# Performance work log

Measured on AMD Instinct MI355X. Metric: run time of the kernel, lower is better.

The kernel has to match this reference:

```python
import jax, jax.numpy as jnp
import numpy as np
import itertools

N_SUBSETS = 4
TAU = 0.1


def setup_inputs() -> dict:
    key = jax.random.key(0)
    k1, k2, k3 = jax.random.split(key, 3)
    # scale projections so exp(sim/tau) stays numerically sane (module assumes small/normalized projections)
    projections = jax.random.normal(k1, (8192, 128), dtype=jnp.float32) * 0.05
    xrecon = jax.random.normal(k2, (8192, 784), dtype=jnp.float32)
    recon_label = jax.random.normal(k3, (8192, 784), dtype=jnp.float32)
    return {"projections": projections, "xrecon": xrecon, "recon_label": recon_label}


def _joint_loss(projections, xrecon, recon_label):
    # reconstruction MSE
    recon_loss = jnp.mean(jnp.square(xrecon - recon_label))

    # ---- XNegloss (SimCLR-style with n_subsets positives per group) ----
    N, D = projections.shape
    sim = (projections @ projections.T) / TAU  # [N, N] dot similarity
    gid = jnp.arange(N) // N_SUBSETS
    pos_mask = gid[:, None] == gid[None, :]  # same-group entries are positives
    exp_sim = jnp.exp(sim)
    # original code drops positive entries exactly equal to 1 (positives[positives != 1])
    pos_sum = jnp.sum(jnp.where(pos_mask & (sim != 1.0), exp_sim, 0.0), axis=-1)
    neg_sum = jnp.sum(jnp.where(pos_mask, 0.0, exp_sim), axis=-1)
    closs = jnp.mean(-jnp.log(pos_sum / (pos_sum + neg_sum)))

    # ---- distance loss: MSE over all subset pairs within each group ----
    combi = np.array(list(itertools.combinations(range(N_SUBSETS), 2)))
    left, right = combi[:, 0], combi[:, 1]
    P = projections.reshape(N // N_SUBSETS, N_SUBSETS, D)
    # per-group mean over (pairs, D) then mean over groups == global mean (equal counts)
    dist_loss = jnp.mean(jnp.square(P[:, left] - P[:, right]))

    loss = recon_loss + closs + dist_loss
    return loss, closs, recon_loss, dist_loss


def reference(projections, xrecon, recon_label):
    return _joint_loss(projections, xrecon, recon_label)
```

## Files before the change

### kernel.cpp

```cpp
#include <hip/hip_runtime.h>
#include <hip/hip_bf16.h>
#include <stdint.h>

typedef __bf16 bf16x8 __attribute__((ext_vector_type(8)));
typedef float  f32x4  __attribute__((ext_vector_type(4)));

#define NROWS   8192
#define DIMK    128
#define RECON_N 6422528
#define RECON_BLOCKS 1568
#define GROUP_BLOCKS 512
#define SIM_TILES    2080
#define FUSED_BLOCKS 4160

#define WS_RS     0
#define WS_G      8192
#define WS_E      16384
#define WS_RPART  24576
#define WS_DPART  26144
#define WS_PB     26656

__device__ __forceinline__ void async16(const void* g, void* l) {
    __builtin_amdgcn_global_load_lds(
        (const __attribute__((address_space(1))) void*)g,
        (__attribute__((address_space(3))) void*)l, 16, 0, 0);
}

__device__ __forceinline__ unsigned short f2bf(float f) {
    union { __hip_bfloat16 h; unsigned short u; } v;
    v.h = __float2bfloat16(f);
    return v.u;
}

__global__ __launch_bounds__(256) void prep_kernel(const float4* __restrict__ Pf,
                                                   uint2* __restrict__ Pb,
                                                   float* __restrict__ ws) {
    int idx = blockIdx.x * 256 + threadIdx.x;
    if (blockIdx.x < 32) ws[WS_RS + idx] = 0.f;
    float4 a = Pf[idx];
    uint2 r;
    r.x = (uint32_t)f2bf(a.x) | ((uint32_t)f2bf(a.y) << 16);
    r.y = (uint32_t)f2bf(a.z) | ((uint32_t)f2bf(a.w) << 16);
    Pb[idx] = r;
}

__global__ __launch_bounds__(256, 3) void fused_kernel(
        const unsigned short* __restrict__ Pb,
        const float* __restrict__ Pf,
        const float4* __restrict__ X,
        const float4* __restrict__ Y,
        float* __restrict__ ws) {
    __shared__ unsigned short tile[128 * 128];
    __shared__ float sred[2][2][64];
    __shared__ float cred[2][128];
    const int bx = blockIdx.x;
    const int wave = threadIdx.x >> 6, lane = threadIdx.x & 63;

    int role, idx;
    if (bx < 4096) {
        int r8 = bx & 7, c8 = bx >> 3;
        if ((r8 & 1) == 0)      { role = 0; idx = c8 * 4 + (r8 >> 1); }
        else if (r8 == 7)       { role = 2; idx = c8; }
        else                    { role = 1; idx = c8 * 3 + ((r8 - 1) >> 1); }
    } else if (bx < 4128) {
        role = 0; idx = 2048 + (bx - 4096);
    } else {
        role = 1; idx = 1536 + (bx - 4128);
    }

    if (role == 0) {
        float* RS = ws + WS_RS;
        float ff = 64.5f - sqrtf(64.5f * 64.5f - 2.0f * (float)idx);
        int I = (int)ff;
        int base = I * 64 - (I * (I - 1)) / 2;
        if (idx < base) { --I; base = I * 64 - (I * (I - 1)) / 2; }
        else { int nb = (I + 1) * 64 - ((I + 1) * I) / 2;
               if (idx >= nb) { ++I; base = nb; } }
        const int J = I + (idx - base);

        const int wr = wave >> 1, wc = wave & 1;
        const int m = lane & 15, kq = lane >> 4;

        const char* gB = (const char*)(Pb + (size_t)J * 128 * DIMK);
#pragma unroll
        for (int i = 0; i < 8; ++i) {
            int chunk = i * 256 + wave * 64 + lane;
            int r = chunk >> 4, qp = chunk & 15;
            async16(gB + r * 256 + (((qp - r) & 15) << 4),
                    (char*)tile + chunk * 16);
        }

        bf16x8 Af[4][4];
        const unsigned short* gA = Pb + (size_t)(I * 128 + wr * 64) * DIMK;
#pragma unroll
        for (int i = 0; i < 4; ++i) {
            const unsigned short* rowp = gA + (size_t)(i * 16 + m) * DIMK + kq * 8;
#pragma unroll
            for (int kk = 0; kk < 4; ++kk)
                Af[i][kk] = *(const bf16x8*)(rowp + kk * 32);
        }

        float rowAcc[4][4];
        float colAcc[4];
#pragma unroll
        for (int i = 0; i < 4; ++i)
#pragma unroll
            for (int r = 0; r < 4; ++r) rowAcc[i][r] = 0.f;

        __syncthreads();

#pragma unroll
        for (int j = 0; j < 4; ++j) {
            int rl = wc * 64 + j * 16 + m;
            bf16x8 Bf[4];
#pragma unroll
            for (int kk = 0; kk < 4; ++kk)
                Bf[kk] = *(const bf16x8*)((const char*)tile + rl * 256 +
                                          (((kq + kk * 4 + rl) & 15) << 4));
            f32x4 acc[4];
#pragma unroll
            for (int i = 0; i < 4; ++i) acc[i] = (f32x4){0.f, 0.f, 0.f, 0.f};
#pragma unroll
            for (int kk = 0; kk < 4; ++kk)
#pragma unroll
                for (int i = 0; i < 4; ++i)
                    acc[i] = __builtin_amdgcn_mfma_f32_16x16x32_bf16(
                        Af[i][kk], Bf[kk], acc[i], 0, 0, 0);
            float cs = 0.f;
#pragma unroll
            for (int i = 0; i < 4; ++i)
#pragma unroll
                for (int r = 0; r < 4; ++r) {
                    float e = __builtin_amdgcn_exp2f(acc[i][r] * 14.426950408889634f);
                    rowAcc[i][r] += e;
                    cs += e;
                }
            cs += __shfl_xor(cs, 16, 64);
            cs += __shfl_xor(cs, 32, 64);
            colAcc[j] = cs;
        }

#pragma unroll
        for (int i = 0; i < 4; ++i)
#pragma unroll
            for (int r = 0; r < 4; ++r) {
                float sv = rowAcc[i][r];
                sv += __shfl_xor(sv, 1, 64);
                sv += __shfl_xor(sv, 2, 64);
                sv += __shfl_xor(sv, 4, 64);
                sv += __shfl_xor(sv, 8, 64);
                rowAcc[i][r] = sv;
            }
        if (m == 0) {
#pragma unroll
            for (int i = 0; i < 4; ++i)
#pragma unroll
                for (int r = 0; r < 4; ++r)
                    sred[wc][wr][i * 16 + kq * 4 + r] = rowAcc[i][r];
        }
        if (kq == 0) {
#pragma unroll
            for (int j = 0; j < 4; ++j)
                cred[wr][wc * 64 + j * 16 + m] = colAcc[j];
        }
        __syncthreads();
        if (wc == 0) {
            float v = sred[0][wr][lane] + sred[1][wr][lane];
            atomicAdd(&RS[I * 128 + wr * 64 + lane], v);
        } else if (I != J) {
            int col = wr * 64 + lane;
            float v = cred[0][col] + cred[1][col];
            atomicAdd(&RS[J * 128 + col], v);
        }
    } else if (role == 1) {
        __shared__ float red[4];
        int base = idx * 1024 + threadIdx.x;
        float4 a0 = X[base],       b0 = Y[base];
        float4 a1 = X[base + 256], b1 = Y[base + 256];
        float4 a2 = X[base + 512], b2 = Y[base + 512];
        float4 a3 = X[base + 768], b3 = Y[base + 768];
        float s = 0.f, d;
        d = a0.x - b0.x; s += d * d;  d = a0.y - b0.y; s += d * d;
        d = a0.z - b0.z; s += d * d;  d = a0.w - b0.w; s += d * d;
        d = a1.x - b1.x; s += d * d;  d = a1.y - b1.y; s += d * d;
        d = a1.z - b1.z; s += d * d;  d = a1.w - b1.w; s += d * d;
        d = a2.x - b2.x; s += d * d;  d = a2.y - b2.y; s += d * d;
        d = a2.z - b2.z; s += d * d;  d = a2.w - b2.w; s += d * d;
        d = a3.x - b3.x; s += d * d;  d = a3.y - b3.y; s += d * d;
        d = a3.z - b3.z; s += d * d;  d = a3.w - b3.w; s += d * d;
#pragma unroll
        for (int mm = 1; mm < 64; mm <<= 1) s += __shfl_xor(s, mm, 64);
        if (lane == 0) red[wave] = s;
        __syncthreads();
        if (threadIdx.x == 0)
            ws[WS_RPART + idx] = red[0] + red[1] + red[2] + red[3];
    } else {
        __shared__ float dred[4];
        float* G = ws + WS_G;
        float* E = ws + WS_E;
        int g = idx * 4 + wave;
        const float* base = Pf + (size_t)g * 4 * DIMK;
        float v[4][2];
#pragma unroll
        for (int r = 0; r < 4; ++r) {
            v[r][0] = base[r * DIMK + lane];
            v[r][1] = base[r * DIMK + 64 + lane];
        }
        float dmat[4][4];
#pragma unroll
        for (int r = 0; r < 4; ++r)
#pragma unroll
            for (int s2 = r; s2 < 4; ++s2) {
                float p = v[r][0] * v[s2][0] + v[r][1] * v[s2][1];
#pragma unroll
                for (int mm = 1; mm < 64; mm <<= 1) p += __shfl_xor(p, mm, 64);
                dmat[r][s2] = p; dmat[s2][r] = p;
            }
        if (lane == 0) {
            float distp = 0.f;
#pragma unroll
            for (int r = 0; r < 4; ++r)
#pragma unroll
                for (int s2 = r + 1; s2 < 4; ++s2)
                    distp += dmat[r][r] + dmat[s2][s2] - 2.f * dmat[r][s2];
            dred[wave] = distp;
#pragma unroll
            for (int r = 0; r < 4; ++r) {
                float Gs = 0.f, Es = 0.f;
#pragma unroll
                for (int s2 = 0; s2 < 4; ++s2) {
                    float sim = dmat[r][s2] * 10.0f;
                    float e = __expf(sim);
                    Gs += e;
                    if (sim == 1.0f) Es += e;
                }
                G[g * 4 + r] = Gs;
                E[g * 4 + r] = Es;
            }
        }
        __syncthreads();
        if (threadIdx.x == 0)
            ws[WS_DPART + idx] = dred[0] + dred[1] + dred[2] + dred[3];
    }
}

__global__ __launch_bounds__(1024) void finalize_kernel(const float* __restrict__ ws,
                                                        float* __restrict__ out) {
    __shared__ float redc[16], redr[16], redd[16];
    const float* RS = ws + WS_RS;
    const float* G  = ws + WS_G;
    const float* E  = ws + WS_E;

    float c = 0.f;
    for (int r = threadIdx.x; r < NROWS; r += 1024) {
        float Sv = RS[r];
        c += __logf(Sv - E[r]) - __logf(G[r] - E[r]);
    }
    float rs = 0.f;
    for (int i = threadIdx.x; i < RECON_BLOCKS; i += 1024) rs += ws[WS_RPART + i];
    float ds = 0.f;
    for (int i = threadIdx.x; i < GROUP_BLOCKS; i += 1024) ds += ws[WS_DPART + i];

#pragma unroll
    for (int mm = 1; mm < 64; mm <<= 1) {
        c  += __shfl_xor(c,  mm, 64);
        rs += __shfl_xor(rs, mm, 64);
        ds += __shfl_xor(ds, mm, 64);
    }
    int wave = threadIdx.x >> 6, lane = threadIdx.x & 63;
    if (lane == 0) { redc[wave] = c; redr[wave] = rs; redd[wave] = ds; }
    __syncthreads();
    if (threadIdx.x == 0) {
        float cs = 0.f, rss = 0.f, dss = 0.f;
#pragma unroll
        for (int i = 0; i < 16; ++i) { cs += redc[i]; rss += redr[i]; dss += redd[i]; }
        float closs = cs / (float)NROWS;
        float recon = rss / (float)RECON_N;
        float dist  = dss / (float)(2048 * 6 * DIMK);
        out[0] = recon + closs + dist;
        out[1] = closs;
        out[2] = recon;
        out[3] = dist;
    }
}

extern "C" void kernel_launch(void* const* d_in, const int* in_sizes, int n_in,
                              void* d_out, int out_size, void* d_ws, size_t ws_size,
                              hipStream_t stream) {
    const float* P  = (const float*)d_in[0];
    const float4* X = (const float4*)d_in[1];
    const float4* Y = (const float4*)d_in[2];
    float* out = (float*)d_out;
    float* w = (float*)d_ws;
    unsigned short* Pb = (unsigned short*)(w + WS_PB);

    prep_kernel<<<1024, 256, 0, stream>>>((const float4*)P, (uint2*)Pb, w);
    fused_kernel<<<FUSED_BLOCKS, 256, 0, stream>>>(Pb, P, X, Y, w);
    finalize_kernel<<<1, 1024, 0, stream>>>(w, out);
}
```

Before: 129.0 us.

## Make fused kernel persistent, interleave recon loads with sim tiles, prefetch next B tile

Replaces the role-partitioned grid of 4160 blocks with a persistent grid of 1024 blocks. Each block loops over similarity tiles, streaming the reconstruction MSE loads in between MFMA steps and staging the next tile's B operand into LDS while the current tile is reduced. The group/distance work moves to the tail of blocks 512 and up. The aim is to hide the memory-bound MSE stream under the compute-bound exp/MFMA work and cut block launch overhead. The cost is more register pressure (occupancy hint raised to 4) and load imbalance, since blocks get either 2 or 3 tiles.

Measured after the change: 161.7 us. 25.3% more time.

```diff
diff --git a/kernel.cpp b/kernel.cpp
--- a/kernel.cpp
+++ b/kernel.cpp
@@ -8,17 +8,16 @@
 #define NROWS   8192
 #define DIMK    128
 #define RECON_N 6422528
-#define RECON_BLOCKS 1568
-#define GROUP_BLOCKS 512
-#define SIM_TILES    2080
-#define FUSED_BLOCKS 4160
+#define NTOT4   1605632
+#define GRID    1024
+#define NTILES  2080
 
 #define WS_RS     0
 #define WS_G      8192
 #define WS_E      16384
 #define WS_RPART  24576
-#define WS_DPART  26144
-#define WS_PB     26656
+#define WS_DPART  25600
+#define WS_PB     26112
 
 __device__ __forceinline__ void async16(const void* g, void* l) {
     __builtin_amdgcn_global_load_lds(
@@ -30,6 +29,28 @@
     union { __hip_bfloat16 h; unsigned short u; } v;
     v.h = __float2bfloat16(f);
     return v.u;
+}
+
+__device__ __forceinline__ void decodeIJ(int u, int& I, int& J) {
+    float ff = 64.5f - sqrtf(64.5f * 64.5f - 2.0f * (float)u);
+    I = (int)ff;
+    int base = I * 64 - (I * (I - 1)) / 2;
+    if (u < base) { --I; base = I * 64 - (I * (I - 1)) / 2; }
+    else { int nb = (I + 1) * 64 - ((I + 1) * I) / 2;
+           if (u >= nb) { ++I; base = nb; } }
+    J = I + (u - base);
+}
+
+__device__ __forceinline__ void stageJ(const unsigned short* Pb, int J,
+                                       unsigned short* tile, int wave, int lane) {
+    const char* gB = (const char*)(Pb + (size_t)J * 128 * DIMK);
+#pragma unroll
+    for (int i = 0; i < 8; ++i) {
+        int chunk = i * 256 + wave * 64 + lane;
+        int r = chunk >> 4, qp = chunk & 15;
+        async16(gB + r * 256 + (((qp - r) & 15) << 4),
+                (char*)tile + chunk * 16);
+    }
 }
 
 __global__ __launch_bounds__(256) void prep_kernel(const float4* __restrict__ Pf,
@@ -44,7 +65,7 @@
     Pb[idx] = r;
 }
 
-__global__ __launch_bounds__(256, 3) void fused_kernel(
+__global__ __launch_bounds__(256, 4) void fused_kernel(
         const unsigned short* __restrict__ Pb,
         const float* __restrict__ Pf,
         const float4* __restrict__ X,
@@ -53,42 +74,30 @@
     __shared__ unsigned short tile[128 * 128];
     __shared__ float sred[2][2][64];
     __shared__ float cred[2][128];
-    const int bx = blockIdx.x;
+    __shared__ float red[4];
+    __shared__ float dred[4];
+
+    const int bid = blockIdx.x;
     const int wave = threadIdx.x >> 6, lane = threadIdx.x & 63;
-
-    int role, idx;
-    if (bx < 4096) {
-        int r8 = bx & 7, c8 = bx >> 3;
-        if ((r8 & 1) == 0)      { role = 0; idx = c8 * 4 + (r8 >> 1); }
-        else if (r8 == 7)       { role = 2; idx = c8; }
-        else                    { role = 1; idx = c8 * 3 + ((r8 - 1) >> 1); }
-    } else if (bx < 4128) {
-        role = 0; idx = 2048 + (bx - 4096);
-    } else {
-        role = 1; idx = 1536 + (bx - 4128);
-    }
-
-    if (role == 0) {
-        float* RS = ws + WS_RS;
-        float ff = 64.5f - sqrtf(64.5f * 64.5f - 2.0f * (float)idx);
-        int I = (int)ff;
-        int base = I * 64 - (I * (I - 1)) / 2;
-        if (idx < base) { --I; base = I * 64 - (I * (I - 1)) / 2; }
-        else { int nb = (I + 1) * 64 - ((I + 1) * I) / 2;
-               if (idx >= nb) { ++I; base = nb; } }
-        const int J = I + (idx - base);
-
-        const int wr = wave >> 1, wc = wave & 1;
-        const int m = lane & 15, kq = lane >> 4;
-
-        const char* gB = (const char*)(Pb + (size_t)J * 128 * DIMK);
-#pragma unroll
-        for (int i = 0; i < 8; ++i) {
-            int chunk = i * 256 + wave * 64 + lane;
-            int r = chunk >> 4, qp = chunk & 15;
-            async16(gB + r * 256 + (((qp - r) & 15) << 4),
-                    (char*)tile + chunk * 16);
-        }
+    const int wr = wave >> 1, wc = wave & 1;
+    const int m = lane & 15, kq = lane >> 4;
+    float* RS = ws + WS_RS;
+
+    const int gi = bid * 256 + threadIdx.x;
+    const bool has7 = gi < (NTOT4 - 6 * 262144);
+    float rsum = 0.f;
+    float4 rx0, ry0, rx1, ry1;
+
+    {
+        int I0, J0; decodeIJ(bid, I0, J0);
+        stageJ(Pb, J0, tile, wave, lane);
+    }
+    rx0 = X[gi]; ry0 = Y[gi];
+    __syncthreads();
+
+    int u = bid, k0 = 0;
+    while (u < NTILES) {
+        int I, J; decodeIJ(u, I, J);
 
         bf16x8 Af[4][4];
         const unsigned short* gA = Pb + (size_t)(I * 128 + wr * 64) * DIMK;
@@ -107,10 +116,18 @@
 #pragma unroll
             for (int r = 0; r < 4; ++r) rowAcc[i][r] = 0.f;
 
-        __syncthreads();
-
 #pragma unroll
         for (int j = 0; j < 4; ++j) {
+            const int k = k0 + j;
+            if (k < 6) {
+                int rk = k + 1;
+                int i1 = rk * 262144 + gi;
+                bool use = (rk < 6) | has7;
+                int ii = use ? i1 : gi;
+                if (j & 1) { rx0 = X[ii]; ry0 = Y[ii]; }
+                else       { rx1 = X[ii]; ry1 = Y[ii]; }
+            }
+
             int rl = wc * 64 + j * 16 + m;
             bf16x8 Bf[4];
 #pragma unroll
@@ -138,6 +155,23 @@
             cs += __shfl_xor(cs, 16, 64);
             cs += __shfl_xor(cs, 32, 64);
             colAcc[j] = cs;
+
+            if (k <= 6) {
+                bool use = (k < 6) | has7;
+                float4 a = (j & 1) ? rx1 : rx0;
+                float4 b = (j & 1) ? ry1 : ry0;
+                float dx = use ? a.x - b.x : 0.f; rsum += dx * dx;
+                float dy = use ? a.y - b.y : 0.f; rsum += dy * dy;
+                float dz = use ? a.z - b.z : 0.f; rsum += dz * dz;
+                float dw = use ? a.w - b.w : 0.f; rsum += dw * dw;
+            }
+        }
+
+        __syncthreads();
+        int un = u + GRID;
+        if (un < NTILES) {
+            int In, Jn; decodeIJ(un, In, Jn);
+            stageJ(Pb, Jn, tile, wave, lane);
         }
 
 #pragma unroll
@@ -172,33 +206,13 @@
             float v = cred[0][col] + cred[1][col];
             atomicAdd(&RS[J * 128 + col], v);
         }
-    } else if (role == 1) {
-        __shared__ float red[4];
-        int base = idx * 1024 + threadIdx.x;
-        float4 a0 = X[base],       b0 = Y[base];
-        float4 a1 = X[base + 256], b1 = Y[base + 256];
-        float4 a2 = X[base + 512], b2 = Y[base + 512];
-        float4 a3 = X[base + 768], b3 = Y[base + 768];
-        float s = 0.f, d;
-        d = a0.x - b0.x; s += d * d;  d = a0.y - b0.y; s += d * d;
-        d = a0.z - b0.z; s += d * d;  d = a0.w - b0.w; s += d * d;
-        d = a1.x - b1.x; s += d * d;  d = a1.y - b1.y; s += d * d;
-        d = a1.z - b1.z; s += d * d;  d = a1.w - b1.w; s += d * d;
-        d = a2.x - b2.x; s += d * d;  d = a2.y - b2.y; s += d * d;
-        d = a2.z - b2.z; s += d * d;  d = a2.w - b2.w; s += d * d;
-        d = a3.x - b3.x; s += d * d;  d = a3.y - b3.y; s += d * d;
-        d = a3.z - b3.z; s += d * d;  d = a3.w - b3.w; s += d * d;
-#pragma unroll
-        for (int mm = 1; mm < 64; mm <<= 1) s += __shfl_xor(s, mm, 64);
-        if (lane == 0) red[wave] = s;
-        __syncthreads();
-        if (threadIdx.x == 0)
-            ws[WS_RPART + idx] = red[0] + red[1] + red[2] + red[3];
-    } else {
-        __shared__ float dred[4];
+        u = un; k0 += 4;
+    }
+
+    if (bid >= 512) {
         float* G = ws + WS_G;
         float* E = ws + WS_E;
-        int g = idx * 4 + wave;
+        int g = (bid - 512) * 4 + wave;
         const float* base = Pf + (size_t)g * 4 * DIMK;
         float v[4][2];
 #pragma unroll
@@ -238,9 +252,16 @@
                 E[g * 4 + r] = Es;
             }
         }
-        __syncthreads();
-        if (threadIdx.x == 0)
-            ws[WS_DPART + idx] = dred[0] + dred[1] + dred[2] + dred[3];
+    }
+
+#pragma unroll
+    for (int mm = 1; mm < 64; mm <<= 1) rsum += __shfl_xor(rsum, mm, 64);
+    if (lane == 0) red[wave] = rsum;
+    __syncthreads();
+    if (threadIdx.x == 0) {
+        ws[WS_RPART + bid] = red[0] + red[1] + red[2] + red[3];
+        if (bid >= 512)
+            ws[WS_DPART + (bid - 512)] = dred[0] + dred[1] + dred[2] + dred[3];
     }
 }
 
@@ -257,9 +278,9 @@
         c += __logf(Sv - E[r]) - __logf(G[r] - E[r]);
     }
     float rs = 0.f;
-    for (int i = threadIdx.x; i < RECON_BLOCKS; i += 1024) rs += ws[WS_RPART + i];
+    for (int i = threadIdx.x; i < GRID; i += 1024) rs += ws[WS_RPART + i];
     float ds = 0.f;
-    for (int i = threadIdx.x; i < GROUP_BLOCKS; i += 1024) ds += ws[WS_DPART + i];
+    for (int i = threadIdx.x; i < 512; i += 1024) ds += ws[WS_DPART + i];
 
 #pragma unroll
     for (int mm = 1; mm < 64; mm <<= 1) {
@@ -295,6 +316,6 @@
     unsigned short* Pb = (unsigned short*)(w + WS_PB);
 
     prep_kernel<<<1024, 256, 0, stream>>>((const float4*)P, (uint2*)Pb, w);
-    fused_kernel<<<FUSED_BLOCKS, 256, 0, stream>>>(Pb, P, X, Y, w);
+    fused_kernel<<<GRID, 256, 0, stream>>>(Pb, P, X, Y, w);
     finalize_kernel<<<1, 1024, 0, stream>>>(w, out);
 }
```

## Move recon MSE streaming into prep kernel, leaving sim kernel compute-only

Applied to the files above, without the earlier changes.

Moves the reconstruction-MSE partial sums out of the fused similarity kernel and into the bf16 conversion prep kernel, forming a streaming kernel. The similarity kernel now interleaves only tile blocks and group-distance blocks in a 4:1 pattern. The aim is to keep each kernel homogeneous, with memory-bound streaming in one and MFMA tiles in the other. In exchange, the recon memory traffic no longer overlaps with the matmul compute.

Measured after the change: 121.6 us. -5.7%, faster.

```diff
diff --git a/kernel.cpp b/kernel.cpp
--- a/kernel.cpp
+++ b/kernel.cpp
@@ -8,10 +8,12 @@
 #define NROWS   8192
 #define DIMK    128
 #define RECON_N 6422528
+#define NTOT4   1605632
 #define RECON_BLOCKS 1568
 #define GROUP_BLOCKS 512
-#define SIM_TILES    2080
-#define FUSED_BLOCKS 4160
+#define NTILES  2080
+#define K1_BLOCKS 2592
+#define K2_BLOCKS 2592
 
 #define WS_RS     0
 #define WS_G      8192
@@ -32,40 +34,68 @@
     return v.u;
 }
 
-__global__ __launch_bounds__(256) void prep_kernel(const float4* __restrict__ Pf,
-                                                   uint2* __restrict__ Pb,
-                                                   float* __restrict__ ws) {
-    int idx = blockIdx.x * 256 + threadIdx.x;
-    if (blockIdx.x < 32) ws[WS_RS + idx] = 0.f;
-    float4 a = Pf[idx];
-    uint2 r;
-    r.x = (uint32_t)f2bf(a.x) | ((uint32_t)f2bf(a.y) << 16);
-    r.y = (uint32_t)f2bf(a.z) | ((uint32_t)f2bf(a.w) << 16);
-    Pb[idx] = r;
-}
-
-__global__ __launch_bounds__(256, 3) void fused_kernel(
+__global__ __launch_bounds__(256) void stream_kernel(
+        const float4* __restrict__ Pf,
+        uint2* __restrict__ Pb,
+        const float4* __restrict__ X,
+        const float4* __restrict__ Y,
+        float* __restrict__ ws) {
+    __shared__ float red[4];
+    const int bid = blockIdx.x;
+    const int wave = threadIdx.x >> 6, lane = threadIdx.x & 63;
+
+    if (bid < 1024) {
+        int idx = bid * 256 + threadIdx.x;
+        if (bid < 32) ws[WS_RS + idx] = 0.f;
+        float4 a = Pf[idx];
+        uint2 r;
+        r.x = (uint32_t)f2bf(a.x) | ((uint32_t)f2bf(a.y) << 16);
+        r.y = (uint32_t)f2bf(a.z) | ((uint32_t)f2bf(a.w) << 16);
+        Pb[idx] = r;
+        return;
+    }
+
+    const int idx = bid - 1024;
+    int base = idx * 1024 + threadIdx.x;
+    float4 a0 = X[base],       b0 = Y[base];
+    float4 a1 = X[base + 256], b1 = Y[base + 256];
+    float4 a2 = X[base + 512], b2 = Y[base + 512];
+    float4 a3 = X[base + 768], b3 = Y[base + 768];
+    float s = 0.f, d;
+    d = a0.x - b0.x; s += d * d;  d = a0.y - b0.y; s += d * d;
+    d = a0.z - b0.z; s += d * d;  d = a0.w - b0.w; s += d * d;
+    d = a1.x - b1.x; s += d * d;  d = a1.y - b1.y; s += d * d;
+    d = a1.z - b1.z; s += d * d;  d = a1.w - b1.w; s += d * d;
+    d = a2.x - b2.x; s += d * d;  d = a2.y - b2.y; s += d * d;
+    d = a2.z - b2.z; s += d * d;  d = a2.w - b2.w; s += d * d;
+    d = a3.x - b3.x; s += d * d;  d = a3.y - b3.y; s += d * d;
+    d = a3.z - b3.z; s += d * d;  d = a3.w - b3.w; s += d * d;
+#pragma unroll
+    for (int mm = 1; mm < 64; mm <<= 1) s += __shfl_xor(s, mm, 64);
+    if (lane == 0) red[wave] = s;
+    __syncthreads();
+    if (threadIdx.x == 0)
+        ws[WS_RPART + idx] = red[0] + red[1] + red[2] + red[3];
+}
+
+__global__ __launch_bounds__(256, 3) void sim_kernel(
         const unsigned short* __restrict__ Pb,
         const float* __restrict__ Pf,
-        const float4* __restrict__ X,
-        const float4* __restrict__ Y,
         float* __restrict__ ws) {
     __shared__ unsigned short tile[128 * 128];
     __shared__ float sred[2][2][64];
     __shared__ float cred[2][128];
+    __shared__ float dred[4];
     const int bx = blockIdx.x;
     const int wave = threadIdx.x >> 6, lane = threadIdx.x & 63;
 
     int role, idx;
-    if (bx < 4096) {
-        int r8 = bx & 7, c8 = bx >> 3;
-        if ((r8 & 1) == 0)      { role = 0; idx = c8 * 4 + (r8 >> 1); }
-        else if (r8 == 7)       { role = 2; idx = c8; }
-        else                    { role = 1; idx = c8 * 3 + ((r8 - 1) >> 1); }
-    } else if (bx < 4128) {
-        role = 0; idx = 2048 + (bx - 4096);
+    if (bx < 2560) {
+        int r5 = bx % 5, c5 = bx / 5;
+        if (r5 == 4) { role = 1; idx = c5; }
+        else         { role = 0; idx = c5 * 4 + r5; }
     } else {
-        role = 1; idx = 1536 + (bx - 4128);
+        role = 0; idx = 2048 + (bx - 2560);
     }
 
     if (role == 0) {
@@ -172,30 +202,7 @@
             float v = cred[0][col] + cred[1][col];
             atomicAdd(&RS[J * 128 + col], v);
         }
-    } else if (role == 1) {
-        __shared__ float red[4];
-        int base = idx * 1024 + threadIdx.x;
-        float4 a0 = X[base],       b0 = Y[base];
-        float4 a1 = X[base + 256], b1 = Y[base + 256];
-        float4 a2 = X[base + 512], b2 = Y[base + 512];
-        float4 a3 = X[base + 768], b3 = Y[base + 768];
-        float s = 0.f, d;
-        d = a0.x - b0.x; s += d * d;  d = a0.y - b0.y; s += d * d;
-        d = a0.z - b0.z; s += d * d;  d = a0.w - b0.w; s += d * d;
-        d = a1.x - b1.x; s += d * d;  d = a1.y - b1.y; s += d * d;
-        d = a1.z - b1.z; s += d * d;  d = a1.w - b1.w; s += d * d;
-        d = a2.x - b2.x; s += d * d;  d = a2.y - b2.y; s += d * d;
-        d = a2.z - b2.z; s += d * d;  d = a2.w - b2.w; s += d * d;
-        d = a3.x - b3.x; s += d * d;  d = a3.y - b3.y; s += d * d;
-        d = a3.z - b3.z; s += d * d;  d = a3.w - b3.w; s += d * d;
-#pragma unroll
-        for (int mm = 1; mm < 64; mm <<= 1) s += __shfl_xor(s, mm, 64);
-        if (lane == 0) red[wave] = s;
-        __syncthreads();
-        if (threadIdx.x == 0)
-            ws[WS_RPART + idx] = red[0] + red[1] + red[2] + red[3];
     } else {
-        __shared__ float dred[4];
         float* G = ws + WS_G;
         float* E = ws + WS_E;
         int g = idx * 4 + wave;
@@ -294,7 +301,8 @@
     float* w = (float*)d_ws;
     unsigned short* Pb = (unsigned short*)(w + WS_PB);
 
-    prep_kernel<<<1024, 256, 0, stream>>>((const float4*)P, (uint2*)Pb, w);
-    fused_kernel<<<FUSED_BLOCKS, 256, 0, stream>>>(Pb, P, X, Y, w);
+    stream_kernel<<<K1_BLOCKS, 256, 0, stream>>>((const float4*)P, (uint2*)Pb,
+                                                 X, Y, w);
+    sim_kernel<<<K2_BLOCKS, 256, 0, stream>>>(Pb, P, w);
     finalize_kernel<<<1, 1024, 0, stream>>>(w, out);
 }
```
